# Kernel tuning notes

Hardware: AMD Instinct MI355X
Metric: run time of the kernel (lower is better)

Reference implementation:

```python
import jax, jax.numpy as jnp
import numpy as np

B, T, D = 2, 2048, 2048
H, HD = 8, 128
C = H * HD  # 1024 channels
BT = 64     # chunk size
EPS_RMS = 1.1920929e-07  # torch fp32 finfo eps (RMSNorm default)


def causal_dw_conv(x, w, b):
    # x: [B,T,C], w: [C,4], b: [C]. Equals torch Conv1d(groups=C, k=4, padding=3)[..., :T]
    Bx, Tx, Cx = x.shape
    xp = jnp.pad(x, ((0, 0), (3, 0), (0, 0)))
    out = sum(xp[:, j:j + Tx, :] * w[None, None, :, j] for j in range(4))
    return out + b


def chunk_kda(q, k, v, g):
    # q,k,g: [B,H,T,K]; v: [B,H,T,V]
    Bx, Hx, Tx, K = q.shape
    V = v.shape[-1]
    NT = Tx // BT
    resh = lambda a: a.reshape(Bx, Hx, NT, BT, a.shape[-1])
    q, k, v, g = map(resh, (q, k, v, g))
    gc = jnp.cumsum(g, axis=-2)                        # [B,H,NT,BT,K]
    diff = gc[..., :, None, :] - gc[..., None, :, :]   # [B,H,NT,BT,BT,K]
    tri_incl = jnp.tril(jnp.ones((BT, BT), bool))
    tri_strict = jnp.tril(jnp.ones((BT, BT), bool), -1)
    Aqk = jnp.einsum('bhnik,bhnjk,bhnijk->bhnij', q, k, jnp.exp(diff)) * tri_incl
    Akk = jnp.einsum('bhnik,bhnjk,bhnijk->bhnij', k, k, jnp.exp(-diff)) * tri_strict
    # UT transform: the in-place forward substitution in the source computes
    # A = (I + strictly_lower(Akk))^{-1}; apply it via a unit-lower triangular solve.
    M = Akk + jnp.eye(BT, dtype=q.dtype)
    rhs = jnp.concatenate([jnp.exp(gc) * k, v], axis=-1)
    sol = jax.scipy.linalg.solve_triangular(M, rhs, lower=True, unit_diagonal=True)
    w_, u = sol[..., :K], sol[..., K:]                 # w = A@(exp(gc)*k), u = A@v
    qg = q * jnp.exp(gc)

    def step(S, xs):
        qg_i, k_i, u_i, gc_i, w_i, Aqk_i = xs
        o_i = qg_i @ S + Aqk_i @ (u_i - w_i @ S)
        g_last = gc_i[:, :, -1]                        # [B,H,K]
        decay = jnp.exp(g_last[:, :, None, :] - gc_i)  # [B,H,BT,K]
        S = S * jnp.exp(g_last)[..., :, None] + jnp.einsum('bhck,bhcv->bhkv', k_i * decay, u_i)
        return S, o_i

    xs = tuple(jnp.moveaxis(a, 2, 0) for a in (qg, k, u, gc, w_, Aqk))
    S0 = jnp.zeros((Bx, Hx, K, V), q.dtype)
    S, o = jax.lax.scan(step, S0, xs)
    o = jnp.moveaxis(o, 0, 2).reshape(Bx, Hx, Tx, V)
    return o, S


def _forward(x, Wq, Wk, Wv, conv_q_w, conv_q_b, conv_k_w, conv_k_b, conv_v_w, conv_v_b,
             Wad, Wau, Wb, Wgd, Wgu, norm_w, Wo):
    Bx, Tx, Dx = x.shape
    heads = lambda y: y.reshape(Bx, Tx, H, HD).transpose(0, 2, 1, 3)
    q = heads(causal_dw_conv(x @ Wq, conv_q_w, conv_q_b))
    k = heads(causal_dw_conv(x @ Wk, conv_k_w, conv_k_b))
    q = q / jnp.maximum(jnp.linalg.norm(q, axis=-1, keepdims=True), 1e-12)
    k = k / jnp.maximum(jnp.linalg.norm(k, axis=-1, keepdims=True), 1e-12)
    v = heads(jax.nn.silu(causal_dw_conv(x @ Wv, conv_v_w, conv_v_b)))
    alpha = jax.nn.sigmoid(heads(x @ Wad @ Wau))
    g = jnp.log(jnp.clip(alpha, 1e-6, None))
    _beta = jax.nn.sigmoid(x @ Wb)  # computed in source but unused by chunk_kda
    o, S = chunk_kda(q, k, v, g)
    o = o.transpose(0, 2, 1, 3)                        # [B,T,H,HD]
    o = o * jax.lax.rsqrt(jnp.mean(o * o, axis=-1, keepdims=True) + EPS_RMS) * norm_w
    gate = jax.nn.sigmoid(x @ Wgd @ Wgu).reshape(Bx, Tx, H, HD)
    o = (o * gate).reshape(Bx, Tx, H * HD)
    return o @ Wo, S


def setup_inputs():
    key = jax.random.key(0)
    ks = jax.random.split(key, 16)
    n = lambda k, shape, s=0.02: jax.random.normal(k, shape, jnp.float32) * s
    return {
        'x': jax.random.normal(ks[0], (B, T, D), jnp.float32),
        'Wq': n(ks[1], (D, C)), 'Wk': n(ks[2], (D, C)), 'Wv': n(ks[3], (D, C)),
        'conv_q_w': n(ks[4], (C, 4), 0.1), 'conv_q_b': jnp.zeros((C,), jnp.float32),
        'conv_k_w': n(ks[5], (C, 4), 0.1), 'conv_k_b': jnp.zeros((C,), jnp.float32),
        'conv_v_w': n(ks[6], (C, 4), 0.1), 'conv_v_b': jnp.zeros((C,), jnp.float32),
        'Wad': n(ks[7], (D, HD)), 'Wau': n(ks[8], (HD, C)),
        'Wb': n(ks[9], (D, H)),
        'Wgd': n(ks[10], (D, HD)), 'Wgu': n(ks[11], (HD, C)),
        'norm_w': jnp.ones((HD,), jnp.float32),
        'Wo': n(ks[12], (C, D)),
    }


def reference(x, Wq, Wk, Wv, conv_q_w, conv_q_b, conv_k_w, conv_k_b, conv_v_w, conv_v_b,
              Wad, Wau, Wb, Wgd, Wgu, norm_w, Wo):
    return _forward(x, Wq, Wk, Wv, conv_q_w, conv_q_b, conv_k_w, conv_k_b, conv_v_w, conv_v_b,
                    Wad, Wau, Wb, Wgd, Wgu, norm_w, Wo)
```

## Files before the change

kernel.cpp:

```cpp
#include <hip/hip_runtime.h>
#include <hip/hip_bf16.h>
#include <cstdint>
#include <cstddef>

constexpr int B_  = 2;
constexpr int T_  = 2048;
constexpr int D_  = 2048;
constexpr int H_  = 8;
constexpr int HD_ = 128;
constexpr int C_  = 1024;
constexpr int BT_ = 64;
constexpr int NT_ = 32;
constexpr int M_  = 4096;
constexpr float EPS_RMS = 1.1920929e-07f;

typedef __bf16 bf16x8 __attribute__((ext_vector_type(8)));
typedef float f32x4 __attribute__((ext_vector_type(4)));

typedef const __attribute__((address_space(1))) unsigned int* gptr_t;
typedef __attribute__((address_space(3))) unsigned int* lptr_t;

__device__ __forceinline__ void gload16(const void* g, void* l) {
  __builtin_amdgcn_global_load_lds((gptr_t)g, (lptr_t)l, 16, 0, 0);
}


#define LD_A(base, mq, dst) do { \
    _Pragma("unroll") for (int i_ = 0; i_ < 4; ++i_) \
      _Pragma("unroll") for (int k_ = 0; k_ < 2; ++k_) \
        dst[i_][k_] = *(const bf16x8*)((base) + (mq) * 8192 + i_ * 2048 + k_ * 1024); \
  } while (0)

#define LD_B(base, nq, dst) do { \
    _Pragma("unroll") for (int j_ = 0; j_ < 2; ++j_) \
      _Pragma("unroll") for (int k_ = 0; k_ < 2; ++k_) \
        dst[j_][k_] = *(const bf16x8*)((base) + (nq) * 4096 + j_ * 2048 + k_ * 1024); \
  } while (0)

#define MM_Q(afr, bfr, mq, nq) do { \
    _Pragma("unroll") for (int i_ = 0; i_ < 4; ++i_) \
      _Pragma("unroll") for (int j_ = 0; j_ < 2; ++j_) \
        _Pragma("unroll") for (int k_ = 0; k_ < 2; ++k_) \
          acc[(mq) * 4 + i_][(nq) * 2 + j_] = __builtin_amdgcn_mfma_f32_16x16x32_bf16( \
              afr[i_][k_], bfr[j_][k_], acc[(mq) * 4 + i_][(nq) * 2 + j_], 0, 0, 0); \
  } while (0)

#define STAGE(src, grow0, kc, loff) do { \
    gload16((src) + (size_t)((grow0) + sr0) * 2048 + (kc) + sc0, smem + (loff) + tid * 16); \
    gload16((src) + (size_t)((grow0) + sr1) * 2048 + (kc) + sc1, smem + (loff) + 8192 + tid * 16); \
  } while (0)

#define PH_SYNC_PRE do { \
    __builtin_amdgcn_s_barrier(); \
    asm volatile("s_waitcnt lgkmcnt(0)" ::: "memory"); \
    __builtin_amdgcn_sched_barrier(0); \
    __builtin_amdgcn_s_setprio(1); \
  } while (0)

#define PH_SYNC_POST do { \
    __builtin_amdgcn_s_setprio(0); \
    __builtin_amdgcn_sched_barrier(0); \
    __builtin_amdgcn_s_barrier(); \
  } while (0)

#define PH_SYNC_POST_VM4 do { \
    __builtin_amdgcn_s_setprio(0); \
    __builtin_amdgcn_sched_barrier(0); \
    asm volatile("s_waitcnt vmcnt(4)" ::: "memory"); \
    __builtin_amdgcn_s_barrier(); \
  } while (0)

#define PH_SYNC_POST_VM0 do { \
    __builtin_amdgcn_s_setprio(0); \
    __builtin_amdgcn_sched_barrier(0); \
    asm volatile("s_waitcnt vmcnt(0)" ::: "memory"); \
    __builtin_amdgcn_s_barrier(); \
  } while (0)

__global__ __launch_bounds__(512, 1) void gemm8p(
    const __hip_bfloat16* __restrict__ A_, const __hip_bfloat16* __restrict__ B_,
    __hip_bfloat16* __restrict__ pre, __hip_bfloat16* __restrict__ adb,
    __hip_bfloat16* __restrict__ gdb) {
  __shared__ alignas(16) char smem[131072];
  const int tid = threadIdx.x, lane = tid & 63;
  const int wid = tid >> 6;
  const int wm = (wid >> 2) * 128, wn = (wid & 3) * 64;
  const int lr = lane & 15, lg = lane >> 4;

  const int bid = blockIdx.x;
  const int swz = (bid & 7) * 26 + (bid >> 3);
  const int mt = swz / 13, nt = swz % 13;
  const int m0 = mt * 256, n0g = nt * 256;

  int ob0 = tid * 16;         ob0 ^= ((ob0 >> 9) & 1) << 5;
  int ob1 = (tid + 512) * 16; ob1 ^= ((ob1 >> 9) & 1) << 5;
  const int sr0 = ((ob0 >> 11) << 4) + ((ob0 >> 6) & 15);
  const int sc0 = ((ob0 >> 10) & 1) * 32 + ((ob0 & 63) >> 1);
  const int sr1 = ((ob1 >> 11) << 4) + ((ob1 >> 6) & 15);
  const int sc1 = ((ob1 >> 10) & 1) * 32 + ((ob1 & 63) >> 1);

  const int foff = lr * 64 + ((lg * 16) ^ ((lr & 8) << 2));
  const int bq = (wn & 64) * 128;
  const char* a0base = smem + (wm >> 7) * 16384 + foff;
  const char* a1base = smem + 65536 + (wm >> 7) * 16384 + foff;
  const char* b0base = smem + 32768 + (wn >> 7) * 16384 + bq + foff;
  const char* b1base = smem + 98304 + (wn >> 7) * 16384 + bq + foff;

  f32x4 acc[8][4];
#pragma unroll
  for (int i = 0; i < 8; ++i)
#pragma unroll
    for (int j = 0; j < 4; ++j) acc[i][j] = (f32x4)(0.f);

  bf16x8 a[4][2], b01[2][2], b23[2][2];

  STAGE(A_, m0,        0, 0);
  STAGE(A_, m0 + 128,  0, 16384);
  STAGE(B_, n0g,       0, 32768);
  STAGE(B_, n0g + 128, 0, 32768 + 16384);
  STAGE(B_, n0g,       64, 98304);
  STAGE(B_, n0g + 128, 64, 98304 + 16384);
  asm volatile("s_waitcnt vmcnt(4)" ::: "memory");
  __builtin_amdgcn_s_barrier();

#pragma unroll 1
  for (int it = 0; it < 15; ++it) {
    const int kA1 = (2 * it + 1) * 64;
    const int kN2 = (2 * it + 2) * 64;
    const int kB3 = (2 * it + 3) * 64;
    LD_A(a0base, 0, a);
    LD_B(b0base, 0, b01);
    STAGE(A_, m0, kA1, 65536);
    PH_SYNC_PRE; MM_Q(a, b01, 0, 0); PH_SYNC_POST;
    LD_B(b0base, 1, b23);
    STAGE(A_, m0 + 128, kA1, 65536 + 16384);
    PH_SYNC_PRE; MM_Q(a, b23, 0, 1); PH_SYNC_POST;
    LD_A(a0base, 1, a);
    STAGE(B_, n0g, kN2, 32768);
    PH_SYNC_PRE; MM_Q(a, b23, 1, 1); PH_SYNC_POST;
    STAGE(B_, n0g + 128, kN2, 32768 + 16384);
    PH_SYNC_PRE; MM_Q(a, b01, 1, 0); PH_SYNC_POST_VM4;
    LD_A(a1base, 0, a);
    LD_B(b1base, 0, b01);
    STAGE(A_, m0, kN2, 0);
    PH_SYNC_PRE; MM_Q(a, b01, 0, 0); PH_SYNC_POST;
    LD_B(b1base, 1, b23);
    STAGE(A_, m0 + 128, kN2, 16384);
    PH_SYNC_PRE; MM_Q(a, b23, 0, 1); PH_SYNC_POST;
    LD_A(a1base, 1, a);
    STAGE(B_, n0g, kB3, 98304);
    PH_SYNC_PRE; MM_Q(a, b23, 1, 1); PH_SYNC_POST;
    STAGE(B_, n0g + 128, kB3, 98304 + 16384);
    PH_SYNC_PRE; MM_Q(a, b01, 1, 0); PH_SYNC_POST_VM4;
  }

  {
    const int kT = 1984;
    LD_A(a0base, 0, a);
    LD_B(b0base, 0, b01);
    STAGE(A_, m0, kT, 65536);
    PH_SYNC_PRE; MM_Q(a, b01, 0, 0); PH_SYNC_POST;
    LD_B(b0base, 1, b23);
    STAGE(A_, m0 + 128, kT, 65536 + 16384);
    PH_SYNC_PRE; MM_Q(a, b23, 0, 1); PH_SYNC_POST;
    LD_A(a0base, 1, a);
    PH_SYNC_PRE; MM_Q(a, b23, 1, 1); PH_SYNC_POST;
    PH_SYNC_PRE; MM_Q(a, b01, 1, 0); PH_SYNC_POST_VM0;
    LD_A(a1base, 0, a);
    LD_B(b1base, 0, b01);
    MM_Q(a, b01, 0, 0);
    LD_B(b1base, 1, b23);
    MM_Q(a, b23, 0, 1);
    LD_A(a1base, 1, a);
    MM_Q(a, b23, 1, 1);
    MM_Q(a, b01, 1, 0);
  }

#pragma unroll
  for (int mf = 0; mf < 8; ++mf) {
    const int row0 = m0 + wm + mf * 16 + lg * 4;
#pragma unroll
    for (int nf = 0; nf < 4; ++nf) {
      const int c = n0g + wn + nf * 16 + lr;
#pragma unroll
      for (int r = 0; r < 4; ++r) {
        const __hip_bfloat16 v = __float2bfloat16(acc[mf][nf][r]);
        const size_t rr = (size_t)(row0 + r);
        if (c < 3072)      pre[rr * 3072 + c] = v;
        else if (c < 3200) adb[rr * 128 + (c - 3072)] = v;
        else               gdb[rr * 128 + (c - 3200)] = v;
      }
    }
  }
}

template <typename OutT>
__global__ __launch_bounds__(256) void gemm_bf16k(
    const __hip_bfloat16* __restrict__ A, const __hip_bfloat16* __restrict__ Bt,
    OutT* __restrict__ C, int N, int K) {
  __shared__ __hip_bfloat16 sA[128 * 32];
  __shared__ __hip_bfloat16 sB[128 * 32];
  const int tid = threadIdx.x;
  const int lane = tid & 63;
  const int m0 = blockIdx.y * 128, n0 = blockIdx.x * 128;
  const int wm = ((tid >> 6) >> 1) * 64, wn = ((tid >> 6) & 1) * 64;
  f32x4 acc[4][4];
#pragma unroll
  for (int i = 0; i < 4; ++i)
#pragma unroll
    for (int j = 0; j < 4; ++j) acc[i][j] = (f32x4)(0.f);
  const int f0 = tid, f1 = tid + 256;
  const int r0 = f0 >> 2, c0 = (f0 & 3) * 8;
  const int r1 = f1 >> 2, c1 = (f1 & 3) * 8;
  const size_t aoff0 = (size_t)(m0 + r0) * K + c0;
  const size_t aoff1 = (size_t)(m0 + r1) * K + c1;
  const size_t boff0 = (size_t)(n0 + r0) * K + c0;
  const size_t boff1 = (size_t)(n0 + r1) * K + c1;
  const int lr = lane & 15, lk = (lane >> 4) * 8;
  for (int k0 = 0; k0 < K; k0 += 32) {
    __syncthreads();
    gload16(A + aoff0 + k0, &sA[f0 * 8]);
    gload16(A + aoff1 + k0, &sA[f1 * 8]);
    gload16(Bt + boff0 + k0, &sB[f0 * 8]);
    gload16(Bt + boff1 + k0, &sB[f1 * 8]);
    __syncthreads();
    bf16x8 af[4], bfr[4];
#pragma unroll
    for (int i = 0; i < 4; ++i)
      af[i] = *(const bf16x8*)&sA[(wm + i * 16 + lr) * 32 + lk];
#pragma unroll
    for (int j = 0; j < 4; ++j)
      bfr[j] = *(const bf16x8*)&sB[(wn + j * 16 + lr) * 32 + lk];
#pragma unroll
    for (int i = 0; i < 4; ++i)
#pragma unroll
      for (int j = 0; j < 4; ++j)
        acc[i][j] = __builtin_amdgcn_mfma_f32_16x16x32_bf16(af[i], bfr[j], acc[i][j], 0, 0, 0);
  }
  const int er = (lane >> 4) * 4, ec = lane & 15;
#pragma unroll
  for (int i = 0; i < 4; ++i) {
#pragma unroll
    for (int j = 0; j < 4; ++j) {
      int row = m0 + wm + i * 16 + er;
      int col = n0 + wn + j * 16 + ec;
#pragma unroll
      for (int r = 0; r < 4; ++r) {
        float v = acc[i][j][r];
        if constexpr (sizeof(OutT) == 2)
          C[(size_t)(row + r) * N + col] = __float2bfloat16(v);
        else
          C[(size_t)(row + r) * N + col] = v;
      }
    }
  }
}

__global__ __launch_bounds__(256) void gemm_augu(
    const __hip_bfloat16* __restrict__ ad, const __hip_bfloat16* __restrict__ gd,
    const __hip_bfloat16* __restrict__ Wau, const __hip_bfloat16* __restrict__ Wgu,
    float* __restrict__ gc, float* __restrict__ glast,
    __hip_bfloat16* __restrict__ gatef) {
  constexpr int N = 1024, K = 128;
  __shared__ alignas(16) char smraw[128 * 132 * 4];
  __hip_bfloat16* sA = (__hip_bfloat16*)smraw;
  __hip_bfloat16* sB = (__hip_bfloat16*)(smraw + 8192);
  float (*scan)[132] = (float(*)[132])smraw;

  const int z = blockIdx.z;
  const __hip_bfloat16* A = z ? gd : ad;
  const __hip_bfloat16* Bt = z ? Wgu : Wau;
  const int tid = threadIdx.x;
  const int lane = tid & 63;
  const int m0 = blockIdx.y * 128, n0 = blockIdx.x * 128;
  const int wm = ((tid >> 6) >> 1) * 64, wn = ((tid >> 6) & 1) * 64;
  f32x4 acc[4][4];
#pragma unroll
  for (int i = 0; i < 4; ++i)
#pragma unroll
    for (int j = 0; j < 4; ++j) acc[i][j] = (f32x4)(0.f);
  const int f0 = tid, f1 = tid + 256;
  const int r0 = f0 >> 2, c0 = (f0 & 3) * 8;
  const int r1 = f1 >> 2, c1 = (f1 & 3) * 8;
  const size_t aoff0 = (size_t)(m0 + r0) * K + c0;
  const size_t aoff1 = (size_t)(m0 + r1) * K + c1;
  const size_t boff0 = (size_t)(n0 + r0) * K + c0;
  const size_t boff1 = (size_t)(n0 + r1) * K + c1;
  const int lr = lane & 15, lk = (lane >> 4) * 8;
#pragma unroll
  for (int k0 = 0; k0 < K; k0 += 32) {
    __syncthreads();
    gload16(A + aoff0 + k0, &sA[f0 * 8]);
    gload16(A + aoff1 + k0, &sA[f1 * 8]);
    gload16(Bt + boff0 + k0, &sB[f0 * 8]);
    gload16(Bt + boff1 + k0, &sB[f1 * 8]);
    __syncthreads();
    bf16x8 af[4], bfr[4];
#pragma unroll
    for (int i = 0; i < 4; ++i)
      af[i] = *(const bf16x8*)&sA[(wm + i * 16 + lr) * 32 + lk];
#pragma unroll
    for (int j = 0; j < 4; ++j)
      bfr[j] = *(const bf16x8*)&sB[(wn + j * 16 + lr) * 32 + lk];
#pragma unroll
    for (int i = 0; i < 4; ++i)
#pragma unroll
      for (int j = 0; j < 4; ++j)
        acc[i][j] = __builtin_amdgcn_mfma_f32_16x16x32_bf16(af[i], bfr[j], acc[i][j], 0, 0, 0);
  }
  const int er = (lane >> 4) * 4, ec = lane & 15;
  if (z == 1) {
#pragma unroll
    for (int i = 0; i < 4; ++i)
#pragma unroll
      for (int j = 0; j < 4; ++j) {
        int row = m0 + wm + i * 16 + er;
        int col = n0 + wn + j * 16 + ec;
#pragma unroll
        for (int r = 0; r < 4; ++r)
          gatef[(size_t)(row + r) * N + col] = __float2bfloat16(acc[i][j][r]);
      }
    return;
  }
  __syncthreads();
#pragma unroll
  for (int i = 0; i < 4; ++i)
#pragma unroll
    for (int j = 0; j < 4; ++j) {
      int rowL = wm + i * 16 + er;
      int colL = wn + j * 16 + ec;
#pragma unroll
      for (int r = 0; r < 4; ++r) {
        float a = acc[i][j][r];
        float s = fmaxf(1.f / (1.f + __expf(-a)), 1e-6f);
        scan[rowL + r][colL] = __logf(s);
      }
    }
  __syncthreads();
  {
    const int d = tid & 127, c2 = tid >> 7;
    const int h = blockIdx.x;
    const int b = m0 >> 11, tb = m0 & 2047;
    const int bh = b * H_ + h;
    float run = 0.f;
    const size_t gbase = ((size_t)bh * T_ + tb + c2 * 64) * 128 + d;
    for (int r = 0; r < 64; ++r) {
      run += scan[c2 * 64 + r][d];
      gc[gbase + (size_t)r * 128] = run;
    }
    glast[((size_t)(bh * NT_ + (tb >> 6) + c2)) * 128 + d] = run;
  }
}

__global__ __launch_bounds__(256) void prep(
    const float* __restrict__ x, const float* __restrict__ Wq,
    const float* __restrict__ Wk, const float* __restrict__ Wv,
    const float* __restrict__ Wad, const float* __restrict__ Wgd,
    const float* __restrict__ Wau, const float* __restrict__ Wgu,
    const float* __restrict__ Wo, __hip_bfloat16* __restrict__ xb,
    __hip_bfloat16* __restrict__ Wt_qkv, __hip_bfloat16* __restrict__ Wt_dg,
    __hip_bfloat16* __restrict__ Wt_aug, __hip_bfloat16* __restrict__ Wt_o) {
  __shared__ float tile[32][33];
  int bid = blockIdx.x;
  const int tid = threadIdx.x;
  if (bid < 8192) {
    size_t i = ((size_t)bid * 256 + tid) * 4;
    float4 v = *(const float4*)(x + i);
    union { __hip_bfloat16 hx[4]; uint2 u2; } pk_;
    pk_.hx[0] = __float2bfloat16(v.x);
    pk_.hx[1] = __float2bfloat16(v.y);
    pk_.hx[2] = __float2bfloat16(v.z);
    pk_.hx[3] = __float2bfloat16(v.w);
    *(uint2*)(xb + i) = pk_.u2;
    return;
  }
  bid -= 8192;
  const float* W; __hip_bfloat16* dst; int K, N, bx, by;
  if (bid < 6144) {
    int z = bid / 2048, r = bid % 2048;
    W = (z == 0) ? Wq : (z == 1) ? Wk : Wv;
    dst = Wt_qkv + (size_t)z * C_ * D_;
    K = D_; N = C_; bx = r & 31; by = r >> 5;
  } else if (bid < 6144 + 512) {
    int b2 = bid - 6144;
    int z = b2 >> 8, r = b2 & 255;
    W = z ? Wgd : Wad;
    dst = Wt_dg + (size_t)z * HD_ * D_;
    K = D_; N = HD_; bx = r & 3; by = r >> 2;
  } else if (bid < 6144 + 512 + 256) {
    int b2 = bid - 6144 - 512;
    int z = b2 >> 7, r = b2 & 127;
    W = z ? Wgu : Wau;
    dst = Wt_aug + (size_t)z * C_ * HD_;
    K = HD_; N = C_; bx = r & 31; by = r >> 5;
  } else {
    int b2 = bid - 6144 - 512 - 256;
    W = Wo; dst = Wt_o;
    K = C_; N = D_; bx = b2 & 63; by = b2 >> 6;
  }
  int tx = tid & 31, ty = tid >> 5;
  int kb = by * 32, nb = bx * 32;
#pragma unroll
  for (int s = 0; s < 4; ++s) {
    int kk = ty + s * 8;
    tile[kk][tx] = W[(size_t)(kb + kk) * N + nb + tx];
  }
  __syncthreads();
#pragma unroll
  for (int s = 0; s < 4; ++s) {
    int nn = ty + s * 8;
    dst[(size_t)(nb + nn) * K + kb + tx] = __float2bfloat16(tile[tx][nn]);
  }
}

__global__ __launch_bounds__(256) void conv_qkv(
    const __hip_bfloat16* __restrict__ pre, const float* __restrict__ gc,
    const float* __restrict__ cqw, const float* __restrict__ cqb,
    const float* __restrict__ ckw, const float* __restrict__ ckb,
    const float* __restrict__ cvw, const float* __restrict__ cvb,
    __hip_bfloat16* __restrict__ qg, __hip_bfloat16* __restrict__ kp,
    __hip_bfloat16* __restrict__ km, __hip_bfloat16* __restrict__ vb) {
  const int bhn = blockIdx.x;
  const int b = bhn >> 8, h = (bhn >> 5) & 7, n = bhn & 31;
  const int wv = threadIdx.x >> 6, lane = threadIdx.x & 63;
  const int d0 = lane * 2;
  const int c0 = h * HD_ + d0;

  float qw[2][4], kw[2][4], vw[2][4], qb2[2], kb2[2], vb2[2];
#pragma unroll
  for (int e = 0; e < 2; ++e) {
    const int c = c0 + e;
#pragma unroll
    for (int j = 0; j < 4; ++j) {
      qw[e][j] = cqw[c * 4 + j];
      kw[e][j] = ckw[c * 4 + j];
      vw[e][j] = cvw[c * 4 + j];
    }
    qb2[e] = cqb[c]; kb2[e] = ckb[c]; vb2[e] = cvb[c];
  }

  const int tw0 = n * 64 + wv * 16;
  const size_t prow0 = ((size_t)b * T_ + tw0) * (3 * C_) + c0;

  float xm[3][3][2];
#pragma unroll
  for (int a = 0; a < 3; ++a)
#pragma unroll
    for (int g2 = 0; g2 < 3; ++g2) { xm[a][g2][0] = 0.f; xm[a][g2][1] = 0.f; }
#pragma unroll
  for (int g2 = 1; g2 <= 3; ++g2) {
    if (tw0 - g2 >= 0) {
      const __hip_bfloat16* pr = pre + (prow0 - (size_t)g2 * (3 * C_));
#pragma unroll
      for (int a = 0; a < 3; ++a) {
        uint u = *(const uint*)(pr + a * C_);
        xm[a][g2 - 1][0] = __bfloat162float(((const __hip_bfloat16*)&u)[0]);
        xm[a][g2 - 1][1] = __bfloat162float(((const __hip_bfloat16*)&u)[1]);
      }
    }
  }

#pragma unroll
  for (int i = 0; i < 16; ++i) {
    const int t = tw0 + i;
    const __hip_bfloat16* pr = pre + (prow0 + (size_t)i * (3 * C_));
    float x0[3][2];
#pragma unroll
    for (int a = 0; a < 3; ++a) {
      uint u = *(const uint*)(pr + a * C_);
      x0[a][0] = __bfloat162float(((const __hip_bfloat16*)&u)[0]);
      x0[a][1] = __bfloat162float(((const __hip_bfloat16*)&u)[1]);
    }
    float aq[2], ak[2], av[2];
#pragma unroll
    for (int e = 0; e < 2; ++e) {
      aq[e] = qb2[e] + qw[e][3] * x0[0][e];
      if (t > 0) aq[e] += qw[e][2] * xm[0][0][e];
      if (t > 1) aq[e] += qw[e][1] * xm[0][1][e];
      if (t > 2) aq[e] += qw[e][0] * xm[0][2][e];
      ak[e] = kb2[e] + kw[e][3] * x0[1][e];
      if (t > 0) ak[e] += kw[e][2] * xm[1][0][e];
      if (t > 1) ak[e] += kw[e][1] * xm[1][1][e];
      if (t > 2) ak[e] += kw[e][0] * xm[1][2][e];
      av[e] = vb2[e] + vw[e][3] * x0[2][e];
      if (t > 0) av[e] += vw[e][2] * xm[2][0][e];
      if (t > 1) av[e] += vw[e][1] * xm[2][1][e];
      if (t > 2) av[e] += vw[e][0] * xm[2][2][e];
    }
#pragma unroll
    for (int a = 0; a < 3; ++a) {
#pragma unroll
      for (int e = 0; e < 2; ++e) {
        xm[a][2][e] = xm[a][1][e];
        xm[a][1][e] = xm[a][0][e];
        xm[a][0][e] = x0[a][e];
      }
    }
    float ssq = aq[0] * aq[0] + aq[1] * aq[1];
    float ssk = ak[0] * ak[0] + ak[1] * ak[1];
#pragma unroll
    for (int o = 1; o < 64; o <<= 1) {
      ssq += __shfl_xor(ssq, o);
      ssk += __shfl_xor(ssk, o);
    }
    const float nq = fmaxf(sqrtf(ssq), 1e-12f);
    const float nk = fmaxf(sqrtf(ssk), 1e-12f);
    const size_t oi = (((size_t)b * H_ + h) * T_ + t) * HD_ + d0;
    const float2 gv = *(const float2*)(gc + oi);
    union { __hip_bfloat16 hx[2]; uint u; } oq, okp, okm, ov;
#pragma unroll
    for (int e = 0; e < 2; ++e) {
      const float g = (e == 0) ? gv.x : gv.y;
      const float eg = __expf(g), emg = __expf(-g);
      oq.hx[e]  = __float2bfloat16(aq[e] / nq * eg);
      const float kn = ak[e] / nk;
      okp.hx[e] = __float2bfloat16(kn * eg);
      okm.hx[e] = __float2bfloat16(kn * emg);
      ov.hx[e]  = __float2bfloat16(av[e] * (1.f / (1.f + __expf(-av[e]))));
    }
    *(uint*)(qg + oi) = oq.u;
    *(uint*)(kp + oi) = okp.u;
    *(uint*)(km + oi) = okm.u;
    *(uint*)(vb + oi) = ov.u;
  }
}

__global__ __launch_bounds__(256) void chunk_mid(
    const __hip_bfloat16* __restrict__ qg, const __hip_bfloat16* __restrict__ kp,
    const __hip_bfloat16* __restrict__ km, const __hip_bfloat16* __restrict__ vb,
    __hip_bfloat16* __restrict__ Aq, __hip_bfloat16* __restrict__ w_bf,
    __hip_bfloat16* __restrict__ u_bf, __hip_bfloat16* __restrict__ PT_bf) {
  __shared__ float A_T[64][68];
  __shared__ float solu[64][128];
  __shared__ __hip_bfloat16 kmS[64 * 128];
  const int tid = threadIdx.x;
  const int bhn = blockIdx.x;
  const size_t gbase = ((size_t)(bhn >> 5) * T_ + (size_t)(bhn & 31) * BT_) * HD_;
  const int wv = tid >> 6, lane = tid & 63;
  const int lr = lane & 15, lg = lane >> 4;
  const int prod = wv >> 1, rh = wv & 1;

  {
    const char* src = (const char*)(km + gbase);
#pragma unroll
    for (int s = 0; s < 4; ++s)
      gload16(src + s * 4096 + tid * 16, ((char*)kmS) + s * 4096 + tid * 16);
  }

  {
    const __hip_bfloat16* A = (prod ? qg : km) + gbase;
    const __hip_bfloat16* Bt = (prod ? km : kp) + gbase;
    f32x4 acc[2][4];
#pragma unroll
    for (int i = 0; i < 2; ++i)
#pragma unroll
      for (int j = 0; j < 4; ++j) acc[i][j] = (f32x4)(0.f);
#pragma unroll
    for (int k0 = 0; k0 < 128; k0 += 32) {
      bf16x8 af[2], bfr[4];
#pragma unroll
      for (int i = 0; i < 2; ++i)
        af[i] = *(const bf16x8*)(A + (size_t)(rh * 32 + i * 16 + lr) * 128 + k0 + lg * 8);
#pragma unroll
      for (int j = 0; j < 4; ++j)
        bfr[j] = *(const bf16x8*)(Bt + (size_t)(j * 16 + lr) * 128 + k0 + lg * 8);
#pragma unroll
      for (int i = 0; i < 2; ++i)
#pragma unroll
        for (int j = 0; j < 4; ++j)
          acc[i][j] = __builtin_amdgcn_mfma_f32_16x16x32_bf16(af[i], bfr[j], acc[i][j], 0, 0, 0);
    }
    if (prod == 0) {
#pragma unroll
      for (int i = 0; i < 2; ++i)
#pragma unroll
        for (int j = 0; j < 4; ++j) {
          int row0 = rh * 32 + i * 16 + lg * 4;
          int col = j * 16 + lr;
          *(float4*)&A_T[col][row0] =
              make_float4(acc[i][j][0], acc[i][j][1], acc[i][j][2], acc[i][j][3]);
        }
    } else {
      __hip_bfloat16* dst = Aq + (size_t)bhn * 4096;
#pragma unroll
      for (int i = 0; i < 2; ++i)
#pragma unroll
        for (int j = 0; j < 4; ++j)
#pragma unroll
          for (int r = 0; r < 4; ++r) {
            int row = rh * 32 + i * 16 + lg * 4 + r;
            int col = j * 16 + lr;
            float v = (col <= row) ? acc[i][j][r] : 0.f;
            dst[row * 64 + col] = __float2bfloat16(v);
          }
    }
  }
  __syncthreads();

  {
    const int col = tid & 127;
    const __hip_bfloat16* rhs = ((tid < 128) ? kp : vb) + gbase;
    float s[64];
#pragma unroll
    for (int i = 0; i < 64; ++i)
      s[i] = __bfloat162float(rhs[(size_t)i * 128 + col]);
#pragma unroll
    for (int ib = 0; ib < 64; ib += 4) {
      const float s0 = s[ib];
      const float s1 = fmaf(-A_T[ib][ib + 1], s0, s[ib + 1]);
      const float s2 = fmaf(-A_T[ib + 1][ib + 2], s1,
                       fmaf(-A_T[ib][ib + 2], s0, s[ib + 2]));
      const float s3 = fmaf(-A_T[ib + 2][ib + 3], s2,
                       fmaf(-A_T[ib + 1][ib + 3], s1,
                       fmaf(-A_T[ib][ib + 3], s0, s[ib + 3])));
      s[ib + 1] = s1; s[ib + 2] = s2; s[ib + 3] = s3;
#pragma unroll
      for (int j4 = ib + 4; j4 < 64; j4 += 4) {
        float4 a0 = *(const float4*)&A_T[ib][j4];
        float4 a1 = *(const float4*)&A_T[ib + 1][j4];
        float4 a2 = *(const float4*)&A_T[ib + 2][j4];
        float4 a3 = *(const float4*)&A_T[ib + 3][j4];
        s[j4]     = fmaf(-a3.x, s3, fmaf(-a2.x, s2, fmaf(-a1.x, s1, fmaf(-a0.x, s0, s[j4]))));
        s[j4 + 1] = fmaf(-a3.y, s3, fmaf(-a2.y, s2, fmaf(-a1.y, s1, fmaf(-a0.y, s0, s[j4 + 1]))));
        s[j4 + 2] = fmaf(-a3.z, s3, fmaf(-a2.z, s2, fmaf(-a1.z, s1, fmaf(-a0.z, s0, s[j4 + 2]))));
        s[j4 + 3] = fmaf(-a3.w, s3, fmaf(-a2.w, s2, fmaf(-a1.w, s1, fmaf(-a0.w, s0, s[j4 + 3]))));
      }
    }
    if (tid < 128) {
#pragma unroll
      for (int i = 0; i < 64; ++i)
        w_bf[gbase + (size_t)i * 128 + col] = __float2bfloat16(s[i]);
    } else {
#pragma unroll
      for (int i = 0; i < 64; ++i) {
        u_bf[gbase + (size_t)i * 128 + col] = __float2bfloat16(s[i]);
        solu[i][col] = s[i];
      }
    }
  }
  __syncthreads();

  {
    const int kd0 = (tid & 15) * 8, vd0 = (tid >> 4) * 8;
    float acc[8][8];
#pragma unroll
    for (int a = 0; a < 8; ++a)
#pragma unroll
      for (int b2 = 0; b2 < 8; ++b2) acc[a][b2] = 0.f;
#pragma unroll 4
    for (int i = 0; i < 64; ++i) {
      uint4 rawv = *(const uint4*)&kmS[i * 128 + kd0];
      const __hip_bfloat16* hp = (const __hip_bfloat16*)&rawv;
      float kv[8];
#pragma unroll
      for (int e = 0; e < 8; ++e) kv[e] = __bfloat162float(hp[e]);
      float uv[8];
      *(float4*)(uv)     = *(const float4*)&solu[i][vd0];
      *(float4*)(uv + 4) = *(const float4*)&solu[i][vd0 + 4];
#pragma unroll
      for (int a = 0; a < 8; ++a)
#pragma unroll
        for (int b2 = 0; b2 < 8; ++b2) acc[a][b2] = fmaf(kv[a], uv[b2], acc[a][b2]);
    }
    __hip_bfloat16* dst = PT_bf + (size_t)bhn * 16384;
#pragma unroll
    for (int b2 = 0; b2 < 8; ++b2) {
      union { __hip_bfloat16 hx[8]; uint4 u4; } pk2;
#pragma unroll
      for (int a = 0; a < 8; ++a) pk2.hx[a] = __float2bfloat16(acc[a][b2]);
      *(uint4*)(dst + (size_t)(vd0 + b2) * 128 + kd0) = pk2.u4;
    }
  }
}

__global__ __launch_bounds__(128) void scan_pt(
    const __hip_bfloat16* __restrict__ PT_bf, const float* __restrict__ glast,
    __hip_bfloat16* __restrict__ STg, float* __restrict__ Sout) {
  int vd = blockIdx.x & 127;
  int bh = blockIdx.x >> 7;
  int kd = threadIdx.x;
  float s = 0.f;
  for (int n = 0; n < NT_; ++n) {
    size_t idx = (((size_t)bh * NT_ + n) * HD_ + vd) * HD_ + kd;
    float p = __bfloat162float(PT_bf[idx]);
    STg[idx] = __float2bfloat16(s);
    float gl = glast[((size_t)bh * NT_ + n) * 128 + kd];
    s = (s + p) * __expf(gl);
  }
  Sout[((size_t)bh * HD_ + kd) * HD_ + vd] = s;
}

__global__ __launch_bounds__(256) void chunk_tail(
    const __hip_bfloat16* __restrict__ qg_bf, const __hip_bfloat16* __restrict__ w_bf,
    const __hip_bfloat16* __restrict__ u_bf, const __hip_bfloat16* __restrict__ Aq_bf,
    const __hip_bfloat16* __restrict__ STg, const __hip_bfloat16* __restrict__ gatef,
    const float* __restrict__ normw, __hip_bfloat16* __restrict__ o2b) {
  constexpr int XTS = 72;
  __shared__ __hip_bfloat16 XT[128 * XTS];
  __shared__ float red[64][4];
  __shared__ __hip_bfloat16 uS[64 * 128];
  const int tid = threadIdx.x;
  const int bhn = blockIdx.x;
  const int bh = bhn >> 5, n = bhn & 31;
  const int b = bh >> 3, h = bh & 7;
  const int t0 = n * 64, hoff = h * 128;
  const size_t gbase = ((size_t)bh * T_ + t0) * 128;
  const __hip_bfloat16* Sg = STg + (size_t)bhn * 16384;

  {
    const char* src = (const char*)(u_bf + gbase);
#pragma unroll
    for (int s = 0; s < 4; ++s)
      gload16(src + s * 4096 + tid * 16, ((char*)uS) + s * 4096 + tid * 16);
  }

  const int wv = tid >> 6, lane = tid & 63;
  const int lr = lane & 15, lg = lane >> 4;
  f32x4 accX[4][2], accO[4][2];
#pragma unroll
  for (int i = 0; i < 4; ++i)
#pragma unroll
    for (int j = 0; j < 2; ++j) { accX[i][j] = (f32x4)(0.f); accO[i][j] = (f32x4)(0.f); }

  const __hip_bfloat16* wrow = w_bf + gbase;
  const __hip_bfloat16* qrow = qg_bf + gbase;
#pragma unroll
  for (int k0 = 0; k0 < 128; k0 += 32) {
    bf16x8 aW[4], aQ[4], bS[2];
#pragma unroll
    for (int i = 0; i < 4; ++i) {
      aW[i] = *(const bf16x8*)(wrow + (size_t)(i * 16 + lr) * 128 + k0 + lg * 8);
      aQ[i] = *(const bf16x8*)(qrow + (size_t)(i * 16 + lr) * 128 + k0 + lg * 8);
    }
#pragma unroll
    for (int j = 0; j < 2; ++j)
      bS[j] = *(const bf16x8*)(Sg + (size_t)(wv * 32 + j * 16 + lr) * 128 + k0 + lg * 8);
#pragma unroll
    for (int i = 0; i < 4; ++i)
#pragma unroll
      for (int j = 0; j < 2; ++j) {
        accX[i][j] = __builtin_amdgcn_mfma_f32_16x16x32_bf16(aW[i], bS[j], accX[i][j], 0, 0, 0);
        accO[i][j] = __builtin_amdgcn_mfma_f32_16x16x32_bf16(aQ[i], bS[j], accO[i][j], 0, 0, 0);
      }
  }

  asm volatile("s_waitcnt vmcnt(0)" ::: "memory");
  __builtin_amdgcn_s_barrier();

#pragma unroll
  for (int i = 0; i < 4; ++i)
#pragma unroll
    for (int j = 0; j < 2; ++j) {
      int row0 = i * 16 + lg * 4;
      int col = wv * 32 + j * 16 + lr;
      union { __hip_bfloat16 hx[4]; uint2 u2; } xv;
#pragma unroll
      for (int r = 0; r < 4; ++r) {
        float uu = __bfloat162float(uS[(row0 + r) * 128 + col]);
        xv.hx[r] = __float2bfloat16(uu - accX[i][j][r]);
      }
      *(uint2*)&XT[col * XTS + row0] = xv.u2;
    }
  __syncthreads();

  const __hip_bfloat16* aqb = Aq_bf + (size_t)bhn * 4096;
#pragma unroll
  for (int k0 = 0; k0 < 64; k0 += 32) {
    bf16x8 aA[4], bX[2];
#pragma unroll
    for (int i = 0; i < 4; ++i)
      aA[i] = *(const bf16x8*)(aqb + (size_t)(i * 16 + lr) * 64 + k0 + lg * 8);
#pragma unroll
    for (int j = 0; j < 2; ++j)
      bX[j] = *(const bf16x8*)&XT[(wv * 32 + j * 16 + lr) * XTS + k0 + lg * 8];
#pragma unroll
    for (int i = 0; i < 4; ++i)
#pragma unroll
      for (int j = 0; j < 2; ++j)
        accO[i][j] = __builtin_amdgcn_mfma_f32_16x16x32_bf16(aA[i], bX[j], accO[i][j], 0, 0, 0);
  }

#pragma unroll
  for (int i = 0; i < 4; ++i)
#pragma unroll
    for (int r = 0; r < 4; ++r) {
      int row = i * 16 + lg * 4 + r;
      float o0 = accO[i][0][r], o1 = accO[i][1][r];
      float ss = o0 * o0 + o1 * o1;
#pragma unroll
      for (int o = 1; o < 16; o <<= 1) ss += __shfl_xor(ss, o);
      if (lr == 0) red[row][wv] = ss;
    }
  __syncthreads();
  float nw0 = normw[wv * 32 + lr];
  float nw1 = normw[wv * 32 + 16 + lr];
#pragma unroll
  for (int i = 0; i < 4; ++i)
#pragma unroll
    for (int r = 0; r < 4; ++r) {
      int row = i * 16 + lg * 4 + r;
      float tot = red[row][0] + red[row][1] + red[row][2] + red[row][3];
      float rms = rsqrtf(tot * (1.f / 128.f) + EPS_RMS);
      size_t orow = (size_t)(b * T_ + t0 + row) * C_ + hoff;
      int c0 = wv * 32 + lr, c1 = c0 + 16;
      float g0 = __bfloat162float(gatef[orow + c0]);
      float g1 = __bfloat162float(gatef[orow + c1]);
      float s0 = 1.f / (1.f + __expf(-g0));
      float s1 = 1.f / (1.f + __expf(-g1));
      o2b[orow + c0] = __float2bfloat16(accO[i][0][r] * rms * nw0 * s0);
      o2b[orow + c1] = __float2bfloat16(accO[i][1][r] * rms * nw1 * s1);
    }
}

extern "C" void kernel_launch(void* const* d_in, const int* in_sizes, int n_in,
                              void* d_out, int out_size, void* d_ws, size_t ws_size,
                              hipStream_t stream) {
  (void)in_sizes; (void)n_in; (void)out_size;
  const float* x    = (const float*)d_in[0];
  const float* Wq   = (const float*)d_in[1];
  const float* Wk   = (const float*)d_in[2];
  const float* Wv   = (const float*)d_in[3];
  const float* cqw  = (const float*)d_in[4];
  const float* cqb  = (const float*)d_in[5];
  const float* ckw  = (const float*)d_in[6];
  const float* ckb  = (const float*)d_in[7];
  const float* cvw  = (const float*)d_in[8];
  const float* cvb  = (const float*)d_in[9];
  const float* Wad  = (const float*)d_in[10];
  const float* Wau  = (const float*)d_in[11];
  const float* Wgd  = (const float*)d_in[13];
  const float* Wgu  = (const float*)d_in[14];
  const float* normw= (const float*)d_in[15];
  const float* Wo   = (const float*)d_in[16];

  float* outp = (float*)d_out;
  float* Sout = outp + (size_t)M_ * D_;

  const size_t SZ = (size_t)M_ * C_;

  float* ws = (float*)d_ws;
  __hip_bfloat16* pre_qkv = (__hip_bfloat16*)(ws);
  float* a_full = ws + 3 * SZ / 2;
  __hip_bfloat16* gatef = (__hip_bfloat16*)(ws + 5 * SZ / 2);
  float* gc_g = ws + 3 * SZ;
  __hip_bfloat16* qg_bf = (__hip_bfloat16*)(ws + 4 * SZ);
  __hip_bfloat16* kp_bf = (__hip_bfloat16*)(ws + 9 * SZ / 2);
  __hip_bfloat16* km_bf = (__hip_bfloat16*)(ws + 5 * SZ);
  __hip_bfloat16* v_bf  = (__hip_bfloat16*)(ws + 11 * SZ / 2);
  __hip_bfloat16* w_bf  = (__hip_bfloat16*)(ws + 6 * SZ);
  __hip_bfloat16* u_bf  = (__hip_bfloat16*)(ws + 13 * SZ / 2);
  __hip_bfloat16* Aq_bf = (__hip_bfloat16*)(ws + 7 * SZ);
  float* glast = ws + 29 * SZ / 4;
  __hip_bfloat16* PT_bf = (__hip_bfloat16*)(ws + 15 * SZ / 2);
  __hip_bfloat16* STg   = (__hip_bfloat16*)(ws + 17 * SZ / 2);
  __hip_bfloat16* xb    = (__hip_bfloat16*)(ws + 19 * SZ / 2);
  __hip_bfloat16* Wt_qkv = (__hip_bfloat16*)(ws + 21 * SZ / 2);
  size_t off = 21 * SZ / 2 + 3 * SZ / 4;
  __hip_bfloat16* Wt_dg  = (__hip_bfloat16*)(ws + off); off += 262144;
  __hip_bfloat16* Wt_aug = (__hip_bfloat16*)(ws + off); off += 131072;
  __hip_bfloat16* Wt_o   = (__hip_bfloat16*)(ws + off); off += 1048576;
  __hip_bfloat16* ad_bf  = (__hip_bfloat16*)(ws + off); off += 262144;
  __hip_bfloat16* gd_bf  = (__hip_bfloat16*)(ws + off); off += 262144;
  if (ws_size < off * sizeof(float)) return;

  __hip_bfloat16* o2b = (__hip_bfloat16*)a_full;
  __hip_bfloat16* Wt_au = Wt_aug;
  __hip_bfloat16* Wt_gu = Wt_aug + (size_t)C_ * HD_;

  prep<<<17152, 256, 0, stream>>>(x, Wq, Wk, Wv, Wad, Wgd, Wau, Wgu, Wo,
                                  xb, Wt_qkv, Wt_dg, Wt_aug, Wt_o);

  gemm8p<<<208, 512, 0, stream>>>(xb, Wt_qkv, pre_qkv, ad_bf, gd_bf);
  gemm_augu<<<dim3(C_ / 128, M_ / 128, 2), 256, 0, stream>>>(
      ad_bf, gd_bf, Wt_au, Wt_gu, gc_g, glast, gatef);

  conv_qkv<<<B_ * H_ * NT_, 256, 0, stream>>>(pre_qkv, gc_g, cqw, cqb, ckw, ckb,
                                              cvw, cvb, qg_bf, kp_bf, km_bf, v_bf);

  chunk_mid<<<B_ * H_ * NT_, 256, 0, stream>>>(qg_bf, kp_bf, km_bf, v_bf,
                                               Aq_bf, w_bf, u_bf, PT_bf);
  scan_pt<<<B_ * H_ * HD_, 128, 0, stream>>>(PT_bf, glast, STg, Sout);

  chunk_tail<<<B_ * H_ * NT_, 256, 0, stream>>>(qg_bf, w_bf, u_bf, Aq_bf, STg,
                                                gatef, normw, o2b);
  gemm_bf16k<float><<<dim3(D_ / 128, M_ / 128), 256, 0, stream>>>(o2b, Wt_o, outp, D_, C_);
}
```

Before: 338.2 us.

## Double threads per block in chunk_mid and chunk_tail with finer wave tiling

Raises chunk_mid and chunk_tail from 256 to 512 threads per block and splits the MFMA tiles across 8 waves, halving each wave's rows or columns. Both kernels launch only 512 blocks, so this is meant to add latency hiding and parallelism per chunk and to cut registers per thread. The triangular solve in chunk_mid still uses only 256 threads, so half the block sits idle during that serial phase.

Result: no change. 340.6 us (+0.7%).

```diff
diff --git a/kernel.cpp b/kernel.cpp
--- a/kernel.cpp
+++ b/kernel.cpp
@@ -525,7 +525,7 @@
   }
 }
 
-__global__ __launch_bounds__(256) void chunk_mid(
+__global__ __launch_bounds__(512) void chunk_mid(
     const __hip_bfloat16* __restrict__ qg, const __hip_bfloat16* __restrict__ kp,
     const __hip_bfloat16* __restrict__ km, const __hip_bfloat16* __restrict__ vb,
     __hip_bfloat16* __restrict__ Aq, __hip_bfloat16* __restrict__ w_bf,
@@ -538,66 +538,56 @@
   const size_t gbase = ((size_t)(bhn >> 5) * T_ + (size_t)(bhn & 31) * BT_) * HD_;
   const int wv = tid >> 6, lane = tid & 63;
   const int lr = lane & 15, lg = lane >> 4;
-  const int prod = wv >> 1, rh = wv & 1;
+  const int prod = wv >> 2, rh = wv & 3;
 
   {
     const char* src = (const char*)(km + gbase);
 #pragma unroll
-    for (int s = 0; s < 4; ++s)
-      gload16(src + s * 4096 + tid * 16, ((char*)kmS) + s * 4096 + tid * 16);
+    for (int s = 0; s < 2; ++s)
+      gload16(src + s * 8192 + tid * 16, ((char*)kmS) + s * 8192 + tid * 16);
   }
 
   {
     const __hip_bfloat16* A = (prod ? qg : km) + gbase;
     const __hip_bfloat16* Bt = (prod ? km : kp) + gbase;
-    f32x4 acc[2][4];
-#pragma unroll
-    for (int i = 0; i < 2; ++i)
-#pragma unroll
-      for (int j = 0; j < 4; ++j) acc[i][j] = (f32x4)(0.f);
+    f32x4 acc[4];
+#pragma unroll
+    for (int j = 0; j < 4; ++j) acc[j] = (f32x4)(0.f);
 #pragma unroll
     for (int k0 = 0; k0 < 128; k0 += 32) {
-      bf16x8 af[2], bfr[4];
-#pragma unroll
-      for (int i = 0; i < 2; ++i)
-        af[i] = *(const bf16x8*)(A + (size_t)(rh * 32 + i * 16 + lr) * 128 + k0 + lg * 8);
+      bf16x8 af, bfr[4];
+      af = *(const bf16x8*)(A + (size_t)(rh * 16 + lr) * 128 + k0 + lg * 8);
 #pragma unroll
       for (int j = 0; j < 4; ++j)
         bfr[j] = *(const bf16x8*)(Bt + (size_t)(j * 16 + lr) * 128 + k0 + lg * 8);
 #pragma unroll
-      for (int i = 0; i < 2; ++i)
-#pragma unroll
-        for (int j = 0; j < 4; ++j)
-          acc[i][j] = __builtin_amdgcn_mfma_f32_16x16x32_bf16(af[i], bfr[j], acc[i][j], 0, 0, 0);
+      for (int j = 0; j < 4; ++j)
+        acc[j] = __builtin_amdgcn_mfma_f32_16x16x32_bf16(af, bfr[j], acc[j], 0, 0, 0);
     }
     if (prod == 0) {
 #pragma unroll
-      for (int i = 0; i < 2; ++i)
-#pragma unroll
-        for (int j = 0; j < 4; ++j) {
-          int row0 = rh * 32 + i * 16 + lg * 4;
-          int col = j * 16 + lr;
-          *(float4*)&A_T[col][row0] =
-              make_float4(acc[i][j][0], acc[i][j][1], acc[i][j][2], acc[i][j][3]);
-        }
+      for (int j = 0; j < 4; ++j) {
+        int row0 = rh * 16 + lg * 4;
+        int col = j * 16 + lr;
+        *(float4*)&A_T[col][row0] =
+            make_float4(acc[j][0], acc[j][1], acc[j][2], acc[j][3]);
+      }
     } else {
       __hip_bfloat16* dst = Aq + (size_t)bhn * 4096;
 #pragma unroll
-      for (int i = 0; i < 2; ++i)
-#pragma unroll
-        for (int j = 0; j < 4; ++j)
-#pragma unroll
-          for (int r = 0; r < 4; ++r) {
-            int row = rh * 32 + i * 16 + lg * 4 + r;
-            int col = j * 16 + lr;
-            float v = (col <= row) ? acc[i][j][r] : 0.f;
-            dst[row * 64 + col] = __float2bfloat16(v);
-          }
+      for (int j = 0; j < 4; ++j)
+#pragma unroll
+        for (int r = 0; r < 4; ++r) {
+          int row = rh * 16 + lg * 4 + r;
+          int col = j * 16 + lr;
+          float v = (col <= row) ? acc[j][r] : 0.f;
+          dst[row * 64 + col] = __float2bfloat16(v);
+        }
     }
   }
   __syncthreads();
 
-  {
+  if (tid < 256) {
     const int col = tid & 127;
     const __hip_bfloat16* rhs = ((tid < 128) ? kp : vb) + gbase;
     float s[64];
@@ -641,12 +631,12 @@
   __syncthreads();
 
   {
-    const int kd0 = (tid & 15) * 8, vd0 = (tid >> 4) * 8;
-    float acc[8][8];
+    const int kd0 = (tid & 15) * 8, vd0 = (tid >> 4) * 4;
+    float acc[8][4];
 #pragma unroll
     for (int a = 0; a < 8; ++a)
 #pragma unroll
-      for (int b2 = 0; b2 < 8; ++b2) acc[a][b2] = 0.f;
+      for (int b2 = 0; b2 < 4; ++b2) acc[a][b2] = 0.f;
 #pragma unroll 4
     for (int i = 0; i < 64; ++i) {
       uint4 rawv = *(const uint4*)&kmS[i * 128 + kd0];
@@ -654,17 +644,18 @@
       float kv[8];
 #pragma unroll
       for (int e = 0; e < 8; ++e) kv[e] = __bfloat162float(hp[e]);
-      float uv[8];
-      *(float4*)(uv)     = *(const float4*)&solu[i][vd0];
-      *(float4*)(uv + 4) = *(const float4*)&solu[i][vd0 + 4];
-#pragma unroll
-      for (int a = 0; a < 8; ++a)
-#pragma unroll
-        for (int b2 = 0; b2 < 8; ++b2) acc[a][b2] = fmaf(kv[a], uv[b2], acc[a][b2]);
+      float4 uv = *(const float4*)&solu[i][vd0];
+#pragma unroll
+      for (int a = 0; a < 8; ++a) {
+        acc[a][0] = fmaf(kv[a], uv.x, acc[a][0]);
+        acc[a][1] = fmaf(kv[a], uv.y, acc[a][1]);
+        acc[a][2] = fmaf(kv[a], uv.z, acc[a][2]);
+        acc[a][3] = fmaf(kv[a], uv.w, acc[a][3]);
+      }
     }
     __hip_bfloat16* dst = PT_bf + (size_t)bhn * 16384;
 #pragma unroll
-    for (int b2 = 0; b2 < 8; ++b2) {
+    for (int b2 = 0; b2 < 4; ++b2) {
       union { __hip_bfloat16 hx[8]; uint4 u4; } pk2;
 #pragma unroll
       for (int a = 0; a < 8; ++a) pk2.hx[a] = __float2bfloat16(acc[a][b2]);
@@ -690,7 +681,7 @@
   Sout[((size_t)bh * HD_ + kd) * HD_ + vd] = s;
 }
 
-__global__ __launch_bounds__(256) void chunk_tail(
+__global__ __launch_bounds__(512) void chunk_tail(
     const __hip_bfloat16* __restrict__ qg_bf, const __hip_bfloat16* __restrict__ w_bf,
     const __hip_bfloat16* __restrict__ u_bf, const __hip_bfloat16* __restrict__ Aq_bf,
     const __hip_bfloat16* __restrict__ STg, const __hip_bfloat16* __restrict__ gatef,
@@ -710,15 +701,16 @@
   {
     const char* src = (const char*)(u_bf + gbase);
 #pragma unroll
-    for (int s = 0; s < 4; ++s)
-      gload16(src + s * 4096 + tid * 16, ((char*)uS) + s * 4096 + tid * 16);
+    for (int s = 0; s < 2; ++s)
+      gload16(src + s * 8192 + tid * 16, ((char*)uS) + s * 8192 + tid * 16);
   }
 
   const int wv = tid >> 6, lane = tid & 63;
   const int lr = lane & 15, lg = lane >> 4;
-  f32x4 accX[4][2], accO[4][2];
-#pragma unroll
-  for (int i = 0; i < 4; ++i)
+  const int rowh = wv >> 2, colq = wv & 3;
+  f32x4 accX[2][2], accO[2][2];
+#pragma unroll
+  for (int i = 0; i < 2; ++i)
 #pragma unroll
     for (int j = 0; j < 2; ++j) { accX[i][j] = (f32x4)(0.f); accO[i][j] = (f32x4)(0.f); }
 
@@ -726,17 +718,17 @@
   const __hip_bfloat16* qrow = qg_bf + gbase;
 #pragma unroll
   for (int k0 = 0; k0 < 128; k0 += 32) {
-    bf16x8 aW[4], aQ[4], bS[2];
-#pragma unroll
-    for (int i = 0; i < 4; ++i) {
-      aW[i] = *(const bf16x8*)(wrow + (size_t)(i * 16 + lr) * 128 + k0 + lg * 8);
-      aQ[i] = *(const bf16x8*)(qrow + (size_t)(i * 16 + lr) * 128 + k0 + lg * 8);
+    bf16x8 aW[2], aQ[2], bS[2];
+#pragma unroll
+    for (int i = 0; i < 2; ++i) {
+      aW[i] = *(const bf16x8*)(wrow + (size_t)(rowh * 32 + i * 16 + lr) * 128 + k0 + lg * 8);
+      aQ[i] = *(const bf16x8*)(qrow + (size_t)(rowh * 32 + i * 16 + lr) * 128 + k0 + lg * 8);
     }
 #pragma unroll
     for (int j = 0; j < 2; ++j)
-      bS[j] = *(const bf16x8*)(Sg + (size_t)(wv * 32 + j * 16 + lr) * 128 + k0 + lg * 8);
-#pragma unroll
-    for (int i = 0; i < 4; ++i)
+      bS[j] = *(const bf16x8*)(Sg + (size_t)(colq * 32 + j * 16 + lr) * 128 + k0 + lg * 8);
+#pragma unroll
+    for (int i = 0; i < 2; ++i)
 #pragma unroll
       for (int j = 0; j < 2; ++j) {
         accX[i][j] = __builtin_amdgcn_mfma_f32_16x16x32_bf16(aW[i], bS[j], accX[i][j], 0, 0, 0);
@@ -748,11 +740,11 @@
   __builtin_amdgcn_s_barrier();
 
 #pragma unroll
-  for (int i = 0; i < 4; ++i)
+  for (int i = 0; i < 2; ++i)
 #pragma unroll
     for (int j = 0; j < 2; ++j) {
-      int row0 = i * 16 + lg * 4;
-      int col = wv * 32 + j * 16 + lr;
+      int row0 = rowh * 32 + i * 16 + lg * 4;
+      int col = colq * 32 + j * 16 + lr;
       union { __hip_bfloat16 hx[4]; uint2 u2; } xv;
 #pragma unroll
       for (int r = 0; r < 4; ++r) {
@@ -766,43 +758,43 @@
   const __hip_bfloat16* aqb = Aq_bf + (size_t)bhn * 4096;
 #pragma unroll
   for (int k0 = 0; k0 < 64; k0 += 32) {
-    bf16x8 aA[4], bX[2];
-#pragma unroll
-    for (int i = 0; i < 4; ++i)
-      aA[i] = *(const bf16x8*)(aqb + (size_t)(i * 16 + lr) * 64 + k0 + lg * 8);
+    bf16x8 aA[2], bX[2];
+#pragma unroll
+    for (int i = 0; i < 2; ++i)
+      aA[i] = *(const bf16x8*)(aqb + (size_t)(rowh * 32 + i * 16 + lr) * 64 + k0 + lg * 8);
 #pragma unroll
     for (int j = 0; j < 2; ++j)
-      bX[j] = *(const bf16x8*)&XT[(wv * 32 + j * 16 + lr) * XTS + k0 + lg * 8];
-#pragma unroll
-    for (int i = 0; i < 4; ++i)
+      bX[j] = *(const bf16x8*)&XT[(colq * 32 + j * 16 + lr) * XTS + k0 + lg * 8];
+#pragma unroll
+    for (int i = 0; i < 2; ++i)
 #pragma unroll
       for (int j = 0; j < 2; ++j)
         accO[i][j] = __builtin_amdgcn_mfma_f32_16x16x32_bf16(aA[i], bX[j], accO[i][j], 0, 0, 0);
   }
 
 #pragma unroll
-  for (int i = 0; i < 4; ++i)
+  for (int i = 0; i < 2; ++i)
 #pragma unroll
     for (int r = 0; r < 4; ++r) {
-      int row = i * 16 + lg * 4 + r;
+      int row = rowh * 32 + i * 16 + lg * 4 + r;
       float o0 = accO[i][0][r], o1 = accO[i][1][r];
       float ss = o0 * o0 + o1 * o1;
 #pragma unroll
       for (int o = 1; o < 16; o <<= 1) ss += __shfl_xor(ss, o);
-      if (lr == 0) red[row][wv] = ss;
+      if (lr == 0) red[row][colq] = ss;
     }
   __syncthreads();
-  float nw0 = normw[wv * 32 + lr];
-  float nw1 = normw[wv * 32 + 16 + lr];
-#pragma unroll
-  for (int i = 0; i < 4; ++i)
+  float nw0 = normw[colq * 32 + lr];
+  float nw1 = normw[colq * 32 + 16 + lr];
+#pragma unroll
+  for (int i = 0; i < 2; ++i)
 #pragma unroll
     for (int r = 0; r < 4; ++r) {
-      int row = i * 16 + lg * 4 + r;
+      int row = rowh * 32 + i * 16 + lg * 4 + r;
       float tot = red[row][0] + red[row][1] + red[row][2] + red[row][3];
       float rms = rsqrtf(tot * (1.f / 128.f) + EPS_RMS);
       size_t orow = (size_t)(b * T_ + t0 + row) * C_ + hoff;
-      int c0 = wv * 32 + lr, c1 = c0 + 16;
+      int c0 = colq * 32 + lr, c1 = c0 + 16;
       float g0 = __bfloat162float(gatef[orow + c0]);
       float g1 = __bfloat162float(gatef[orow + c1]);
       float s0 = 1.f / (1.f + __expf(-g0));
@@ -877,11 +869,11 @@
   conv_qkv<<<B_ * H_ * NT_, 256, 0, stream>>>(pre_qkv, gc_g, cqw, cqb, ckw, ckb,
                                               cvw, cvb, qg_bf, kp_bf, km_bf, v_bf);
 
-  chunk_mid<<<B_ * H_ * NT_, 256, 0, stream>>>(qg_bf, kp_bf, km_bf, v_bf,
+  chunk_mid<<<B_ * H_ * NT_, 512, 0, stream>>>(qg_bf, kp_bf, km_bf, v_bf,
                                                Aq_bf, w_bf, u_bf, PT_bf);
   scan_pt<<<B_ * H_ * HD_, 128, 0, stream>>>(PT_bf, glast, STg, Sout);
 
-  chunk_tail<<<B_ * H_ * NT_, 256, 0, stream>>>(qg_bf, w_bf, u_bf, Aq_bf, STg,
+  chunk_tail<<<B_ * H_ * NT_, 512, 0, stream>>>(qg_bf, w_bf, u_bf, Aq_bf, STg,
                                                 gatef, normw, o2b);
   gemm_bf16k<float><<<dim3(D_ / 128, M_ / 128), 256, 0, stream>>>(o2b, Wt_o, outp, D_, C_);
 }
```
